# Performance work log

Hardware: AMD Instinct MI355X
Metric: run time of the kernel (lower is better)

Reference implementation:

```python
import jax, jax.numpy as jnp
import numpy as np

B, H, S, D = 4, 16, 2048, 64


def setup_inputs() -> dict:
    key = jax.random.key(0)
    kq, kk, kv = jax.random.split(key, 3)
    q = jax.random.normal(kq, (B, H, S, D), dtype=jnp.float32)
    k = jax.random.normal(kk, (B, H, S, D), dtype=jnp.float32)
    v = jax.random.normal(kv, (B, H, S, D), dtype=jnp.float32)
    return {"q": q, "k": k, "v": v}


def reference(q, k, v):
    d_k = q.shape[-1]
    scale = 1.0 / jnp.sqrt(jnp.asarray(d_k, dtype=q.dtype))
    # scores: [B, H, S_q, S_k]
    scores = jnp.einsum("bhqd,bhkd->bhqk", q, k) * scale
    attn = jax.nn.softmax(scores, axis=-1)
    out = jnp.einsum("bhqk,bhkd->bhqd", attn, v)
    return out
```

## Files before the change

### kernel.cpp

```cpp
#include <hip/hip_runtime.h>


#define NT 32
#define M0 10.0f

typedef unsigned short u16;
typedef unsigned int   u32;
typedef __bf16 bf16x8 __attribute__((ext_vector_type(8)));
typedef u16    u16x8  __attribute__((ext_vector_type(8)));
typedef u32    u32x4  __attribute__((ext_vector_type(4)));
typedef float  f32x16 __attribute__((ext_vector_type(16)));

__device__ __forceinline__ u16 f2bf(float f) {
    union { float f; u32 u; } x; x.f = f;
    u32 r = x.u + 0x7FFFu + ((x.u >> 16) & 1u);
    return (u16)(r >> 16);
}
__device__ __forceinline__ u32 cvt_pk_bf16(float lo, float hi) {
    u32 r; asm("v_cvt_pk_bf16_f32 %0, %1, %2" : "=v"(r) : "v"(lo), "v"(hi));
    return r;
}
__device__ __forceinline__ float fexp2(float x) {
    float r; asm("v_exp_f32 %0, %1" : "=v"(r) : "v"(x));
    return r;
}

__global__ __launch_bounds__(256)
void prepass_kernel(const float* __restrict__ K, const float* __restrict__ V,
                    u16* __restrict__ Kb, u16* __restrict__ Vt)
{
    __shared__ u16 T[64 * 66];
    const int t   = threadIdx.x;
    const int bh  = blockIdx.x >> 5;
    const int s0  = (blockIdx.x & 31) * 64;
    const int row = t >> 2;
    const int c0  = (t & 3) * 16;

    {
        const float* kp = K + ((size_t)bh * 2048 + s0 + row) * 64 + c0;
        #pragma unroll
        for (int i = 0; i < 2; ++i) {
            float4 a = ((const float4*)kp)[2 * i];
            float4 b = ((const float4*)kp)[2 * i + 1];
            u16x8 o;
            o[0] = f2bf(a.x); o[1] = f2bf(a.y); o[2] = f2bf(a.z); o[3] = f2bf(a.w);
            o[4] = f2bf(b.x); o[5] = f2bf(b.y); o[6] = f2bf(b.z); o[7] = f2bf(b.w);
            *(u16x8*)(Kb + ((size_t)bh * 2048 + s0 + row) * 64 + c0 + 8 * i) = o;
        }
    }
    {
        const float* vp = V + ((size_t)bh * 2048 + s0 + row) * 64 + c0;
        #pragma unroll
        for (int i = 0; i < 4; ++i) {
            float4 a = ((const float4*)vp)[i];
            T[(c0 + 4 * i + 0) * 66 + row] = f2bf(a.x);
            T[(c0 + 4 * i + 1) * 66 + row] = f2bf(a.y);
            T[(c0 + 4 * i + 2) * 66 + row] = f2bf(a.z);
            T[(c0 + 4 * i + 3) * 66 + row] = f2bf(a.w);
        }
    }
    __syncthreads();
    {
        const int d  = t >> 2;
        const int k0 = (t & 3) * 16;
        #pragma unroll
        for (int i = 0; i < 2; ++i) {
            u16x8 o;
            #pragma unroll
            for (int j = 0; j < 8; ++j) o[j] = T[d * 66 + k0 + 8 * i + j];
            *(u16x8*)(Vt + ((size_t)bh * 64 + d) * 2048 + s0 + k0 + 8 * i) = o;
        }
    }
}

__global__ __launch_bounds__(256)
void attn_fwd_kernel(const float* __restrict__ Qg, const u16* __restrict__ Kb,
                     const u16* __restrict__ Vt, float* __restrict__ Og)
{
    __shared__ u16 Klds[2][4096];
    __shared__ u16 Vlds[2][4096];

    const int tid = threadIdx.x;
    const int w   = tid >> 6;
    const int l31 = tid & 31;
    const int hi  = (tid & 63) >> 5;
    const int sw  = l31 & 7;

    const int id = (blockIdx.x & 7) * 128 + (blockIdx.x >> 3);
    const int bh = id >> 4;
    const int q0 = (id & 15) * 128;
    const int qw = q0 + w * 32;
    const int qr = qw + l31;

    const size_t baseQ = (size_t)bh * 2048 * 64;
    const u16* kg = Kb + (size_t)bh * 2048 * 64;
    const u16* vg = Vt + (size_t)bh * 64 * 2048;

    const float SCL = 0.125f * 1.44269504088896f;
    bf16x8 bq[4];
    #pragma unroll
    for (int dc = 0; dc < 4; ++dc) {
        const float* qp = Qg + baseQ + (size_t)qr * 64 + dc * 16 + hi * 8;
        float4 a = ((const float4*)qp)[0];
        float4 b = ((const float4*)qp)[1];
        u16x8 t;
        t[0] = f2bf(a.x * SCL); t[1] = f2bf(a.y * SCL);
        t[2] = f2bf(a.z * SCL); t[3] = f2bf(a.w * SCL);
        t[4] = f2bf(b.x * SCL); t[5] = f2bf(b.y * SCL);
        t[6] = f2bf(b.z * SCL); t[7] = f2bf(b.w * SCL);
        bq[dc] = __builtin_bit_cast(bf16x8, t);
    }

    int co[4];
    #pragma unroll
    for (int c = 0; c < 4; ++c) co[c] = ((2 * c + hi) ^ sw) * 8;

    u32x4 onev; onev[0] = 0x3F803F80u; onev[1] = 0x3F803F80u;
    onev[2] = 0x3F803F80u; onev[3] = 0x3F803F80u;
    const bf16x8 bones = __builtin_bit_cast(bf16x8, onev);

    f32x16 acc[2], acc2;
    #pragma unroll
    for (int i = 0; i < 16; ++i) { acc[0][i] = 0.f; acc[1][i] = 0.f; acc2[i] = 0.f; }

    const int srow = tid >> 3;
    const int kc   = ((tid & 7) ^ (srow & 7)) * 8;
    const u16* kS0 = kg + (size_t)srow * 64 + kc;
    const u16* kS1 = kg + (size_t)(srow + 32) * 64 + kc;
    const u16* vS0 = vg + (size_t)srow * 2048 + kc;
    const u16* vS1 = vg + (size_t)(srow + 32) * 2048 + kc;

    u16x8 rA, rB, rC, rD;
    auto load_tile = [&](int t) {
        rA = *(const u16x8*)(kS0 + (size_t)t * 4096);
        rB = *(const u16x8*)(kS1 + (size_t)t * 4096);
        rC = *(const u16x8*)(vS0 + (size_t)t * 64);
        rD = *(const u16x8*)(vS1 + (size_t)t * 64);
    };
    auto write_tile = [&](int t) {
        u16* kd = &Klds[t & 1][tid * 8];
        u16* vd = &Vlds[t & 1][tid * 8];
        *(u16x8*)kd = rA;
        *(u16x8*)(kd + 2048) = rB;
        *(u16x8*)vd = rC;
        *(u16x8*)(vd + 2048) = rD;
    };

    auto compute = [&](const u16* Kl, const u16* Vl) {
        #pragma unroll
        for (int kh = 0; kh < 2; ++kh) {
            f32x16 s0;
            #pragma unroll
            for (int i = 0; i < 16; ++i) s0[i] = -M0;
            __builtin_amdgcn_s_setprio(1);
            #pragma unroll
            for (int dc = 0; dc < 4; ++dc) {
                bf16x8 ak = *(const bf16x8*)(Kl + (kh * 32 + l31) * 64 + co[dc]);
                s0 = __builtin_amdgcn_mfma_f32_32x32x16_bf16(ak, bq[dc], s0, 0, 0, 0);
            }
            __builtin_amdgcn_s_setprio(0);

            #pragma unroll
            for (int i = 0; i < 16; ++i) s0[i] = fexp2(s0[i]);

            u32 w0[8];
            #pragma unroll
            for (int a = 0; a < 8; ++a)
                w0[a] = cvt_pk_bf16(s0[2 * a], s0[2 * a + 1]);

            __builtin_amdgcn_s_setprio(1);
            #pragma unroll
            for (int ki = 0; ki < 2; ++ki) {
                const int ks = kh * 2 + ki, mb = 4 * ki;
                u32 a0 = w0[mb + 0], a2 = w0[mb + 2];
                u32 a1 = w0[mb + 1], a3 = w0[mb + 3];
                asm("v_permlane32_swap_b32 %0, %1" : "+v"(a0), "+v"(a2));
                asm("v_permlane32_swap_b32 %0, %1" : "+v"(a1), "+v"(a3));
                u32x4 fw0; fw0[0] = a0; fw0[1] = a1; fw0[2] = a2; fw0[3] = a3;
                bf16x8 pa = __builtin_bit_cast(bf16x8, fw0);

                bf16x8 bv0 = *(const bf16x8*)(Vl + l31 * 64 + co[ks]);
                bf16x8 bv1 = *(const bf16x8*)(Vl + (32 + l31) * 64 + co[ks]);
                acc[0] = __builtin_amdgcn_mfma_f32_32x32x16_bf16(pa, bv0, acc[0], 0, 0, 0);
                acc[1] = __builtin_amdgcn_mfma_f32_32x32x16_bf16(pa, bv1, acc[1], 0, 0, 0);
                acc2   = __builtin_amdgcn_mfma_f32_32x32x16_bf16(pa, bones, acc2, 0, 0, 0);
            }
            __builtin_amdgcn_s_setprio(0);
            __builtin_amdgcn_sched_barrier(0);
        }
    };

    load_tile(0);
    write_tile(0);
    __syncthreads();
    for (int t = 0; t < NT; ++t) {
        if (t + 1 < NT) load_tile(t + 1);
        compute(Klds[t & 1], Vlds[t & 1]);
        if (t + 1 < NT) {
            write_tile(t + 1);
            __syncthreads();
        }
    }

    #pragma unroll
    for (int r = 0; r < 16; ++r) {
        int cr = (r & 3) + 8 * (r >> 2) + 4 * hi;
        float inv = 1.0f / acc2[r];
        size_t o = baseQ + (size_t)(qw + cr) * 64 + l31;
        Og[o]      = acc[0][r] * inv;
        Og[o + 32] = acc[1][r] * inv;
    }
}

extern "C" void kernel_launch(void* const* d_in, const int* in_sizes, int n_in,
                              void* d_out, int out_size, void* d_ws, size_t ws_size,
                              hipStream_t stream) {
    const float* q = (const float*)d_in[0];
    const float* k = (const float*)d_in[1];
    const float* v = (const float*)d_in[2];
    float* o = (float*)d_out;
    u16* kb = (u16*)d_ws;
    u16* vt = kb + (size_t)64 * 2048 * 64;
    prepass_kernel<<<dim3(2048), dim3(256), 0, stream>>>(k, v, kb, vt);
    attn_fwd_kernel<<<dim3(1024), dim3(256), 0, stream>>>(q, kb, vt, o);
}
```

Before: 112.9 us.

## Move LDS bank swizzle into prepass global layout and split fragment loads

The XOR swizzle of K and V^T tiles now happens in the prepass, at 4-element granularity with a 16-way mask, so the global bf16 buffers are stored pre-swizzled. The main kernel's tile loads become a plain linear copy into LDS, and each MFMA fragment is read as two 8-byte LDS loads at swizzled offsets instead of one 16-byte load. The sched_barrier between the two kh halves is also removed, giving the compiler more freedom to interleave work. The finer swizzle is meant to reduce LDS bank conflicts, but it doubles the number of LDS read instructions.

New measurement: 121.1 us. +7.2%, slower.

```diff
diff --git a/kernel.cpp b/kernel.cpp
--- a/kernel.cpp
+++ b/kernel.cpp
@@ -8,6 +8,7 @@
 typedef unsigned int   u32;
 typedef __bf16 bf16x8 __attribute__((ext_vector_type(8)));
 typedef u16    u16x8  __attribute__((ext_vector_type(8)));
+typedef u16    u16x4  __attribute__((ext_vector_type(4)));
 typedef u32    u32x4  __attribute__((ext_vector_type(4)));
 typedef float  f32x16 __attribute__((ext_vector_type(16)));
 
@@ -37,15 +38,19 @@
     const int c0  = (t & 3) * 16;
 
     {
-        const float* kp = K + ((size_t)bh * 2048 + s0 + row) * 64 + c0;
-        #pragma unroll
-        for (int i = 0; i < 2; ++i) {
-            float4 a = ((const float4*)kp)[2 * i];
-            float4 b = ((const float4*)kp)[2 * i + 1];
+        const float* kr = K + ((size_t)bh * 2048 + s0 + row) * 64;
+        const int m = row & 15;
+        #pragma unroll
+        for (int h = 0; h < 2; ++h) {
             u16x8 o;
-            o[0] = f2bf(a.x); o[1] = f2bf(a.y); o[2] = f2bf(a.z); o[3] = f2bf(a.w);
-            o[4] = f2bf(b.x); o[5] = f2bf(b.y); o[6] = f2bf(b.z); o[7] = f2bf(b.w);
-            *(u16x8*)(Kb + ((size_t)bh * 2048 + s0 + row) * 64 + c0 + 8 * i) = o;
+            #pragma unroll
+            for (int j = 0; j < 2; ++j) {
+                const int s = (t & 3) * 4 + h * 2 + j;
+                const float4 f = *(const float4*)(kr + ((s ^ m) * 4));
+                o[j * 4 + 0] = f2bf(f.x); o[j * 4 + 1] = f2bf(f.y);
+                o[j * 4 + 2] = f2bf(f.z); o[j * 4 + 3] = f2bf(f.w);
+            }
+            *(u16x8*)(Kb + ((size_t)bh * 2048 + s0 + row) * 64 + c0 + h * 8) = o;
         }
     }
     {
@@ -62,13 +67,18 @@
     __syncthreads();
     {
         const int d  = t >> 2;
-        const int k0 = (t & 3) * 16;
-        #pragma unroll
-        for (int i = 0; i < 2; ++i) {
+        const int md = d & 15;
+        #pragma unroll
+        for (int h = 0; h < 2; ++h) {
             u16x8 o;
             #pragma unroll
-            for (int j = 0; j < 8; ++j) o[j] = T[d * 66 + k0 + 8 * i + j];
-            *(u16x8*)(Vt + ((size_t)bh * 64 + d) * 2048 + s0 + k0 + 8 * i) = o;
+            for (int j = 0; j < 2; ++j) {
+                const int s   = (t & 3) * 4 + h * 2 + j;
+                const int src = (s ^ md) * 4;
+                #pragma unroll
+                for (int i = 0; i < 4; ++i) o[j * 4 + i] = T[d * 66 + src + i];
+            }
+            *(u16x8*)(Vt + ((size_t)bh * 64 + d) * 2048 + s0 + c0 + h * 8) = o;
         }
     }
 }
@@ -84,7 +94,7 @@
     const int w   = tid >> 6;
     const int l31 = tid & 31;
     const int hi  = (tid & 63) >> 5;
-    const int sw  = l31 & 7;
+    const int mlane = l31 & 15;
 
     const int id = (blockIdx.x & 7) * 128 + (blockIdx.x >> 3);
     const int bh = id >> 4;
@@ -111,9 +121,18 @@
         bq[dc] = __builtin_bit_cast(bf16x8, t);
     }
 
-    int co[4];
-    #pragma unroll
-    for (int c = 0; c < 4; ++c) co[c] = ((2 * c + hi) ^ sw) * 8;
+    int po[4];
+    #pragma unroll
+    for (int c = 0; c < 4; ++c) po[c] = ((4 * c + 2 * hi) ^ mlane) * 4;
+
+    auto ldfrag = [&](const u16* rowp, int c) {
+        u16x4 a = *(const u16x4*)(rowp + po[c]);
+        u16x4 b = *(const u16x4*)(rowp + (po[c] ^ 4));
+        u16x8 r;
+        r[0] = a[0]; r[1] = a[1]; r[2] = a[2]; r[3] = a[3];
+        r[4] = b[0]; r[5] = b[1]; r[6] = b[2]; r[7] = b[3];
+        return __builtin_bit_cast(bf16x8, r);
+    };
 
     u32x4 onev; onev[0] = 0x3F803F80u; onev[1] = 0x3F803F80u;
     onev[2] = 0x3F803F80u; onev[3] = 0x3F803F80u;
@@ -124,7 +143,7 @@
     for (int i = 0; i < 16; ++i) { acc[0][i] = 0.f; acc[1][i] = 0.f; acc2[i] = 0.f; }
 
     const int srow = tid >> 3;
-    const int kc   = ((tid & 7) ^ (srow & 7)) * 8;
+    const int kc   = (tid & 7) * 8;
     const u16* kS0 = kg + (size_t)srow * 64 + kc;
     const u16* kS1 = kg + (size_t)(srow + 32) * 64 + kc;
     const u16* vS0 = vg + (size_t)srow * 2048 + kc;
@@ -149,13 +168,14 @@
     auto compute = [&](const u16* Kl, const u16* Vl) {
         #pragma unroll
         for (int kh = 0; kh < 2; ++kh) {
+            const u16* krow = Kl + (kh * 32 + l31) * 64;
             f32x16 s0;
             #pragma unroll
             for (int i = 0; i < 16; ++i) s0[i] = -M0;
             __builtin_amdgcn_s_setprio(1);
             #pragma unroll
             for (int dc = 0; dc < 4; ++dc) {
-                bf16x8 ak = *(const bf16x8*)(Kl + (kh * 32 + l31) * 64 + co[dc]);
+                bf16x8 ak = ldfrag(krow, dc);
                 s0 = __builtin_amdgcn_mfma_f32_32x32x16_bf16(ak, bq[dc], s0, 0, 0, 0);
             }
             __builtin_amdgcn_s_setprio(0);
@@ -179,14 +199,13 @@
                 u32x4 fw0; fw0[0] = a0; fw0[1] = a1; fw0[2] = a2; fw0[3] = a3;
                 bf16x8 pa = __builtin_bit_cast(bf16x8, fw0);
 
-                bf16x8 bv0 = *(const bf16x8*)(Vl + l31 * 64 + co[ks]);
-                bf16x8 bv1 = *(const bf16x8*)(Vl + (32 + l31) * 64 + co[ks]);
+                bf16x8 bv0 = ldfrag(Vl + l31 * 64, ks);
+                bf16x8 bv1 = ldfrag(Vl + (32 + l31) * 64, ks);
                 acc[0] = __builtin_amdgcn_mfma_f32_32x32x16_bf16(pa, bv0, acc[0], 0, 0, 0);
                 acc[1] = __builtin_amdgcn_mfma_f32_32x32x16_bf16(pa, bv1, acc[1], 0, 0, 0);
                 acc2   = __builtin_amdgcn_mfma_f32_32x32x16_bf16(pa, bones, acc2, 0, 0, 0);
             }
             __builtin_amdgcn_s_setprio(0);
-            __builtin_amdgcn_sched_barrier(0);
         }
     };
 
```
